# Performance work log

Measured on AMD Instinct MI355X. Metric: run time of the kernel, lower is better.

## Reference

```python
import jax, jax.numpy as jnp
import numpy as np

# Module config (matches init_kwargs)
RADIUS = 1
N_POINTS = 8
NUM_BINS = 8
DENSITY = True
LBP_MAX = 2 ** N_POINTS - 1  # 255


def _circle_offsets(radius, n_points):
    # skimage local_binary_pattern sampling coordinates:
    # rr = -radius*sin(2*pi*i/P), cc = radius*cos(2*pi*i/P)
    offs = []
    for i in range(n_points):
        ang = 2.0 * np.pi * i / n_points
        dy = -radius * np.sin(ang)
        dx = radius * np.cos(ang)
        # skimage snaps near-integer coords to exact integers (eps rounding)
        if abs(dy - round(dy)) < 1e-8:
            dy = float(round(dy))
        if abs(dx - round(dx)) < 1e-8:
            dx = float(round(dx))
        offs.append((dy, dx))
    return offs


def _bilinear_shift(xp, pad, dy, dx, H, W):
    # Bilinear sample of every pixel's neighbor at constant offset (dy, dx),
    # zero padding outside the image (skimage uses constant-0 border mode).
    fy, fx = int(np.floor(dy)), int(np.floor(dx))
    ty, tx = dy - fy, dx - fx

    def sl(oy, ox):
        return xp[..., pad + oy:pad + oy + H, pad + ox:pad + ox + W]

    return ((1.0 - ty) * (1.0 - tx) * sl(fy, fx)
            + (1.0 - ty) * tx * sl(fy, fx + 1)
            + ty * (1.0 - tx) * sl(fy + 1, fx)
            + ty * tx * sl(fy + 1, fx + 1))


def _lbp_codes(x):
    # x: (B, C, H, W) -> integer-valued LBP codes (B, C, H, W), method='default'
    B, C, H, W = x.shape
    pad = int(np.ceil(RADIUS)) + 1
    xp = jnp.pad(x, ((0, 0), (0, 0), (pad, pad), (pad, pad)))
    code = jnp.zeros(x.shape, dtype=jnp.float32)
    for i, (dy, dx) in enumerate(_circle_offsets(RADIUS, N_POINTS)):
        nb = _bilinear_shift(xp, pad, dy, dx, H, W)
        bit = (nb - x >= 0).astype(jnp.float32)
        code = code + bit * float(2 ** i)
    return code


def _histogram(codes):
    # np.histogram(bins=NUM_BINS, range=(0, LBP_MAX), density=True) per channel
    B, C, H, W = codes.shape
    width = LBP_MAX / NUM_BINS
    idx = jnp.clip((codes * (1.0 / width)).astype(jnp.int32), 0, NUM_BINS - 1)
    idx_flat = idx.reshape(B * C, H * W)
    counts = jax.vmap(
        lambda ix: jnp.zeros((NUM_BINS,), jnp.float32).at[ix].add(1.0)
    )(idx_flat)  # (B*C, NUM_BINS)
    if DENSITY:
        counts = counts / (float(H * W) * width)
    return counts.reshape(B, C, NUM_BINS)


def setup_inputs() -> dict:
    key = jax.random.key(0)
    x = jax.random.normal(key, (32, 3, 512, 512), dtype=jnp.float32)
    return {"x": x}


def reference(x):
    codes = _lbp_codes(x)               # (B, C, H, W)
    hist = _histogram(codes)            # (B, C, NUM_BINS)
    return hist.reshape(hist.shape[0], -1).astype(jnp.float32)  # (B, C*NUM_BINS)
```

## Files before the change

### kernel.cpp

```cpp
#include <hip/hip_runtime.h>

#define W 512
#define H 512
#define CH_PIX (W * H)

__device__ __forceinline__ float2 lr_for(float4 v, float hk, int half, int lane) {
    const float up = __shfl_up(v.w, 1, 64);
    const float dn = __shfl_down(v.x, 1, 64);
    const float eL = half ? hk : 0.0f;
    const float eR = half ? 0.0f : hk;
    float2 r;
    r.x = (lane == 0)  ? eL : up;
    r.y = (lane == 63) ? eR : dn;
    return r;
}

__global__ __launch_bounds__(256, 5) void lbp_main_k(const float* __restrict__ x,
                                                     unsigned int* __restrict__ ws) {
    const int chan = blockIdx.x;
    const int band = blockIdx.y;
    const int tid  = threadIdx.x;
    const int wave  = tid >> 6;
    const int lane  = tid & 63;
    const int strip = wave >> 1;
    const int half  = wave & 1;

    __shared__ unsigned int h[8 * 64];
    for (int i = tid; i < 512; i += 256) h[i] = 0u;
    __syncthreads();

    constexpr double Sd = 0.7071067811865476;
    constexpr double Td = 1.0 - Sd;
    const float wSS = (float)(Sd * Sd);
    const float wST = (float)(Sd * Td);
    const float wTT = (float)(Td * Td);

    const int colbase = half * 256 + (lane << 2);
    const int haloCol = half ? 255 : 256;
    const int cb   = chan * CH_PIX;
    const int y0   = band * 32 + strip * 16;
    const bool lastStrip = (y0 == 496);
    const int base = cb + y0 * W + colbase;

    unsigned long long c64 = 0ull;
    float4 buf[17];

    #pragma unroll
    for (int k = 0; k < 5; ++k) buf[k] = *(const float4*)(x + base + k * W);

    float hvAll = 0.0f;
    {
        int yy = y0 + lane;
        yy = yy > 511 ? 511 : yy;
        if (lane < 17) hvAll = x[cb + yy * W + haloCol];
    }

    #pragma unroll
    for (int k = 5; k < 9; ++k) buf[k] = *(const float4*)(x + base + k * W);

    auto rowpix = [&](const float4& m4, float mL, float mR,
                      const float4& d4, float dL, float dR) {
        const float cs[4]  = {m4.x, m4.y, m4.z, m4.w};
        const float es[4]  = {m4.y, m4.z, m4.w, mR};
        const float wsA[4] = {mL,   m4.x, m4.y, m4.z};
        const float ss[4]  = {d4.x, d4.y, d4.z, d4.w};
        const float sws[4] = {dL,   d4.x, d4.y, d4.z};
        const float ses[4] = {d4.y, d4.z, d4.w, dR};
        #pragma unroll
        for (int i = 0; i < 4; ++i) {
            const float c  = cs[i];
            const float tc = wTT * c;
            const float ts = wST * ss[i];
            const float nb5 = ((wST * wsA[i] + tc) + wSS * sws[i]) + ts;
            const float nb7 = ((tc + wST * es[i]) + ts) + wSS * ses[i];
            const unsigned int amt = (nb5   >= c ? 8u  : 0u)
                                   + (ss[i] >= c ? 16u : 0u)
                                   + (nb7   >= c ? 32u : 0u);
            c64 += 1ull << amt;
        }
    };

    float4 m4  = buf[0];
    float2 mlr = lr_for(m4, __shfl(hvAll, 0, 64), half, lane);

    #define ROWSTEP(k)                                                       \
    {                                                                        \
        float4 d4 = buf[(k) + 1];                                            \
        float dhk = __shfl(hvAll, (k) + 1, 64);                              \
        if (lastStrip && (k) == 15) {                                        \
            d4.x = 0.0f; d4.y = 0.0f; d4.z = 0.0f; d4.w = 0.0f; dhk = 0.0f;  \
        }                                                                    \
        const float2 dlr = lr_for(d4, dhk, half, lane);                      \
        rowpix(m4, mlr.x, mlr.y, d4, dlr.x, dlr.y);                          \
        m4 = d4; mlr = dlr;                                                  \
    }

    ROWSTEP(0) ROWSTEP(1) ROWSTEP(2) ROWSTEP(3)
    #pragma unroll
    for (int k = 9; k < 13; ++k) buf[k] = *(const float4*)(x + base + k * W);
    ROWSTEP(4) ROWSTEP(5) ROWSTEP(6) ROWSTEP(7)
    #pragma unroll
    for (int k = 13; k < 17; ++k) {
        const int kk = (k == 16 && lastStrip) ? 15 : k;
        buf[k] = *(const float4*)(x + base + kk * W);
    }
    ROWSTEP(8) ROWSTEP(9) ROWSTEP(10) ROWSTEP(11)
    ROWSTEP(12) ROWSTEP(13) ROWSTEP(14) ROWSTEP(15)
    #undef ROWSTEP

    const unsigned int lo = (unsigned int)c64;
    const unsigned int hi = (unsigned int)(c64 >> 32);
    #pragma unroll
    for (int b = 0; b < 4; ++b) {
        atomicAdd(&h[(b       << 6) + lane], (lo >> (b * 8)) & 0xffu);
        atomicAdd(&h[((b + 4) << 6) + lane], (hi >> (b * 8)) & 0xffu);
    }
    __syncthreads();

    if (tid < 8) {
        unsigned int s = 0;
        #pragma unroll
        for (int l = 0; l < 64; ++l) s += h[(tid << 6) + l];
        ws[(chan * 16 + band) * 8 + tid] = s;
    }
}

__global__ __launch_bounds__(64) void finalize_k(const unsigned int* __restrict__ ws,
                                                 float* __restrict__ out) {
    const int gid = blockIdx.x * 64 + threadIdx.x;
    if (gid < 768) {
        const int chan = gid >> 3, bin = gid & 7;
        unsigned int s = 0;
        #pragma unroll
        for (int b = 0; b < 16; ++b) s += ws[(chan * 16 + b) * 8 + bin];
        out[gid] = (float)s / 8355840.0f;
    }
}

extern "C" void kernel_launch(void* const* d_in, const int* in_sizes, int n_in,
                              void* d_out, int out_size, void* d_ws, size_t ws_size,
                              hipStream_t stream) {
    const float* x = (const float*)d_in[0];
    unsigned int* wsp = (unsigned int*)d_ws;
    float* out = (float*)d_out;

    dim3 grid(96, 16);
    lbp_main_k<<<grid, 256, 0, stream>>>(x, wsp);
    finalize_k<<<12, 64, 0, stream>>>(wsp, out);
}
```

Before: 33.66 us.

## Issue all row loads upfront, cheaper bin packing, wave-shuffle histogram reduction

```diff
diff --git a/kernel.cpp b/kernel.cpp
--- a/kernel.cpp
+++ b/kernel.cpp
@@ -15,8 +15,8 @@
     return r;
 }
 
-__global__ __launch_bounds__(256, 5) void lbp_main_k(const float* __restrict__ x,
-                                                     unsigned int* __restrict__ ws) {
+__global__ __launch_bounds__(256) void lbp_main_k(const float* __restrict__ x,
+                                                  unsigned int* __restrict__ ws) {
     const int chan = blockIdx.x;
     const int band = blockIdx.y;
     const int tid  = threadIdx.x;
@@ -43,10 +43,15 @@
     const int base = cb + y0 * W + colbase;
 
     unsigned long long c64 = 0ull;
+
     float4 buf[17];
-
     #pragma unroll
-    for (int k = 0; k < 5; ++k) buf[k] = *(const float4*)(x + base + k * W);
+    for (int k = 0; k < 16; ++k) buf[k] = *(const float4*)(x + base + k * W);
+    if (lastStrip) {
+        buf[16].x = 0.0f; buf[16].y = 0.0f; buf[16].z = 0.0f; buf[16].w = 0.0f;
+    } else {
+        buf[16] = *(const float4*)(x + base + 16 * W);
+    }
 
     float hvAll = 0.0f;
     {
@@ -54,9 +59,6 @@
         yy = yy > 511 ? 511 : yy;
         if (lane < 17) hvAll = x[cb + yy * W + haloCol];
     }
-
-    #pragma unroll
-    for (int k = 5; k < 9; ++k) buf[k] = *(const float4*)(x + base + k * W);
 
     auto rowpix = [&](const float4& m4, float mL, float mR,
                       const float4& d4, float dL, float dR) {
@@ -73,40 +75,29 @@
             const float ts = wST * ss[i];
             const float nb5 = ((wST * wsA[i] + tc) + wSS * sws[i]) + ts;
             const float nb7 = ((tc + wST * es[i]) + ts) + wSS * ses[i];
-            const unsigned int amt = (nb5   >= c ? 8u  : 0u)
-                                   + (ss[i] >= c ? 16u : 0u)
-                                   + (nb7   >= c ? 32u : 0u);
-            c64 += 1ull << amt;
+            const bool p0 = (nb5   >= c);
+            const bool p1 = (ss[i] >= c);
+            const bool p2 = (nb7   >= c);
+            unsigned int t = p0 ? 0x100u : 1u;
+            t = p1 ? (t << 16) : t;
+            c64 += (unsigned long long)t << (p2 ? 32 : 0);
         }
     };
 
     float4 m4  = buf[0];
     float2 mlr = lr_for(m4, __shfl(hvAll, 0, 64), half, lane);
 
-    #define ROWSTEP(k)                                                       \
-    {                                                                        \
-        float4 d4 = buf[(k) + 1];                                            \
-        float dhk = __shfl(hvAll, (k) + 1, 64);                              \
-        if (lastStrip && (k) == 15) {                                        \
-            d4.x = 0.0f; d4.y = 0.0f; d4.z = 0.0f; d4.w = 0.0f; dhk = 0.0f;  \
-        }                                                                    \
-        const float2 dlr = lr_for(d4, dhk, half, lane);                      \
-        rowpix(m4, mlr.x, mlr.y, d4, dlr.x, dlr.y);                          \
-        m4 = d4; mlr = dlr;                                                  \
+    #pragma unroll
+    for (int k = 0; k < 16; ++k) {
+        float4 d4 = buf[k + 1];
+        float dhk = __shfl(hvAll, k + 1, 64);
+        if (k == 15 && lastStrip) {
+            d4.x = 0.0f; d4.y = 0.0f; d4.z = 0.0f; d4.w = 0.0f; dhk = 0.0f;
+        }
+        const float2 dlr = lr_for(d4, dhk, half, lane);
+        rowpix(m4, mlr.x, mlr.y, d4, dlr.x, dlr.y);
+        m4 = d4; mlr = dlr;
     }
-
-    ROWSTEP(0) ROWSTEP(1) ROWSTEP(2) ROWSTEP(3)
-    #pragma unroll
-    for (int k = 9; k < 13; ++k) buf[k] = *(const float4*)(x + base + k * W);
-    ROWSTEP(4) ROWSTEP(5) ROWSTEP(6) ROWSTEP(7)
-    #pragma unroll
-    for (int k = 13; k < 17; ++k) {
-        const int kk = (k == 16 && lastStrip) ? 15 : k;
-        buf[k] = *(const float4*)(x + base + kk * W);
-    }
-    ROWSTEP(8) ROWSTEP(9) ROWSTEP(10) ROWSTEP(11)
-    ROWSTEP(12) ROWSTEP(13) ROWSTEP(14) ROWSTEP(15)
-    #undef ROWSTEP
 
     const unsigned int lo = (unsigned int)c64;
     const unsigned int hi = (unsigned int)(c64 >> 32);
@@ -117,11 +108,17 @@
     }
     __syncthreads();
 
-    if (tid < 8) {
-        unsigned int s = 0;
-        #pragma unroll
-        for (int l = 0; l < 64; ++l) s += h[(tid << 6) + l];
-        ws[(chan * 16 + band) * 8 + tid] = s;
+    unsigned int v0 = h[tid];
+    unsigned int v1 = h[tid + 256];
+    #pragma unroll
+    for (int off = 32; off >= 1; off >>= 1) {
+        v0 += __shfl_xor(v0, off, 64);
+        v1 += __shfl_xor(v1, off, 64);
+    }
+    if (lane == 0) {
+        unsigned int* dst = &ws[(chan * 16 + band) * 8];
+        dst[wave]     = v0;
+        dst[wave + 4] = v1;
     }
 }
 
```

Measured after the change: 27.19 us. 19.2% less time.
